# Optimization experiments

Hardware: AMD Instinct MI355X
Metric: run time of the kernel (lower is better)

The kernel has to match this reference:

```python
import jax, jax.numpy as jnp
import numpy as np

B, C_I, C_O, K, H, W = 8, 64, 64, 3, 256, 256
GROUPS = 16  # int(c_o / min(4, c_o)) = 64/4
EPS = 1e-5
PAD = K  # pad_x = pad_y = k + (bc-1) with bc_x=bc_y=1, k=3


def _conv(x, w):
    # x: (B, C_i, h, w), w: (C_o, C_i, K, K), valid conv, stride 1
    return jax.lax.conv_general_dilated(
        x, w, window_strides=(1, 1), padding='VALID',
        dimension_numbers=('NCHW', 'OIHW', 'NCHW'))


def setup_inputs() -> dict:
    key = jax.random.key(0)
    ks = jax.random.split(key, 10)
    s = 1.0 / np.sqrt(C_I * K * K)  # torch Conv2d default init bound
    wshape = (C_O, C_I, K, K)
    names = ['w_int', 'w_tl', 'w_tr', 'w_bl', 'w_br', 'w_top', 'w_bot', 'w_left', 'w_right']
    d = {'x': jax.random.normal(ks[0], (B, C_I, H, W), dtype=jnp.float32)}
    for i, n in enumerate(names):
        d[n] = jax.random.uniform(ks[i + 1], wshape, jnp.float32, -s, s)
    d['bias'] = jnp.zeros((1, C_O, 1, 1), jnp.float32)   # learnable_bias (init zeros)
    d['gamma'] = jnp.ones((C_O,), jnp.float32)           # GroupNorm weight
    d['beta'] = jnp.zeros((C_O,), jnp.float32)           # GroupNorm bias
    return d


def reference(x, w_int, w_tl, w_tr, w_bl, w_br, w_top, w_bot, w_left, w_right, bias, gamma, beta):
    p = PAD
    # corners -> (B,C,1,1)
    tl = _conv(x[:, :, :p, :p], w_tl)
    tr = _conv(x[:, :, :p, -p:], w_tr)
    bl = _conv(x[:, :, -p:, :p], w_bl)
    br = _conv(x[:, :, -p:, -p:], w_br)
    # edges -> (B,C,1,W-2) / (B,C,H-2,1)
    top = _conv(x[:, :, :p, :], w_top)
    bot = _conv(x[:, :, -p:, :], w_bot)
    left = _conv(x[:, :, :, :p], w_left)
    right = _conv(x[:, :, :, -p:], w_right)
    # interior -> (B,C,H-2,W-2)
    mid = _conv(x, w_int)
    mid = jnp.concatenate([left, mid, right], axis=3)       # (B,C,H-2,W)
    top_row = jnp.concatenate([tl, top, tr], axis=3)        # (B,C,1,W)
    bot_row = jnp.concatenate([bl, bot, br], axis=3)        # (B,C,1,W)
    # NOTE: original code puts the 'bottom' conv output first along dim 2
    y = jnp.concatenate([bot_row, mid, top_row], axis=2) + bias  # (B,C,H,W)
    # GroupNorm(16, 64)
    yg = y.reshape(B, GROUPS, -1)
    mu = jnp.mean(yg, axis=2, keepdims=True)
    var = jnp.var(yg, axis=2, keepdims=True)
    yn = ((yg - mu) * jax.lax.rsqrt(var + EPS)).reshape(B, C_O, H, W)
    yn = yn * gamma[None, :, None, None] + beta[None, :, None, None]
    # SELU activation; dropout(rate=0) is identity
    return jax.nn.selu(yn)
```

## Files before the change

kernel.cpp:

```cpp
#include <hip/hip_runtime.h>

#define B_ 8
#define CI 64
#define CO 64
#define H_ 256
#define W_ 256
#define EPS_ 1e-5f

#define SELU_SCALE 1.0507009873554805f
#define SELU_SA    1.7580993408473766f

typedef __attribute__((ext_vector_type(8))) short short8;
typedef __attribute__((ext_vector_type(4))) float f32x4;
typedef unsigned int u32;

__device__ __forceinline__ unsigned short f2bf(float f) {
    unsigned int u = __float_as_uint(f);
    u = (u + 0x7fffu + ((u >> 16) & 1u)) >> 16;
    return (unsigned short)u;
}
__device__ __forceinline__ float bf2f(unsigned short h) {
    return __uint_as_float(((unsigned)h) << 16);
}
__device__ __forceinline__ float selu_f(float u) {
    return (u > 0.f) ? SELU_SCALE * u : SELU_SA * (__expf(u) - 1.f);
}
__device__ __forceinline__ void gload_lds16(const void* g, void* l) {
    __builtin_amdgcn_global_load_lds(
        (const __attribute__((address_space(1))) u32*)g,
        (__attribute__((address_space(3))) u32*)l, 16, 0, 0);
}

__global__ __launch_bounds__(256) void prepass_weights(
    const float* __restrict__ w_int,
    const float* __restrict__ w_bl, const float* __restrict__ w_br,
    const float* __restrict__ w_tl, const float* __restrict__ w_tr,
    const float* __restrict__ w_bot, const float* __restrict__ w_top,
    const float* __restrict__ w_left, const float* __restrict__ w_right,
    unsigned short* __restrict__ wpre9, float* __restrict__ wedge)
{
    const int blk = blockIdx.x, t = threadIdx.x;
    const int wid = blk / 9, pos = blk % 9;
    const float* src = (wid == 0) ? w_bl : (wid == 1) ? w_br
                     : (wid == 2) ? w_tl : (wid == 3) ? w_tr
                     : (wid == 4) ? w_bot : (wid == 5) ? w_top
                     : (wid == 6) ? w_left : (wid == 7) ? w_right : w_int;
    for (int k = 0; k < 16; ++k) {
        const int lin = k * 256 + t;
        const int co = lin >> 6, cip = lin & 63;
        const int ci = cip ^ ((co & 7) << 3);
        wpre9[(size_t)wid * 36864 + pos * 4096 + lin] = f2bf(src[(co * 64 + ci) * 9 + pos]);
        if (wid < 8) {
            const int c4 = lin >> 8, co2 = (lin >> 2) & 63, j = lin & 3;
            const int ci2 = c4 * 4 + j;
            wedge[(size_t)wid * 36864 + pos * 4096 + lin] = src[(co2 * 64 + ci2) * 9 + pos];
        }
    }
}

__global__ __launch_bounds__(256) void prepass_x(
    const float* __restrict__ x, unsigned short* __restrict__ xpre)
{
    __shared__ unsigned short ls[256 * 72];
    const int row = blockIdx.x, b = blockIdx.y;
    const int t = threadIdx.x;
    const int colq = t >> 2;
    const float* xb = x + ((size_t)(b * 64) * 256 + row) * 256;

    for (int sp = 0; sp < 4; ++sp) {
        const int cibase = sp * 16 + (t & 3) * 4;
        float4 v[4];
#pragma unroll
        for (int e = 0; e < 4; ++e)
            v[e] = *(const float4*)(xb + (size_t)(cibase + e) * 65536 + colq * 4);
#pragma unroll
        for (int jj = 0; jj < 4; ++jj) {
            const int col = colq * 4 + jj;
            const int sw  = (col & 7) << 3;
            ushort4 pk;
            pk.x = f2bf((&v[0].x)[jj]);
            pk.y = f2bf((&v[1].x)[jj]);
            pk.z = f2bf((&v[2].x)[jj]);
            pk.w = f2bf((&v[3].x)[jj]);
            *(ushort4*)&ls[col * 72 + (cibase ^ sw)] = pk;
        }
    }
    __syncthreads();
    unsigned short* xp = xpre + ((size_t)(b * 256 + row)) * 256 * 64;
    for (int q = 0; q < 8; ++q) {
        const int lin = q * 256 + t;
        const int col = lin >> 3, k = lin & 7;
        *(uint4*)(xp + col * 64 + k * 8) = *(const uint4*)&ls[col * 72 + k * 8];
    }
}

__global__ __launch_bounds__(512, 4) void conv_mfma(
    const unsigned short* __restrict__ xpre, const unsigned short* __restrict__ wpre,
    const float* __restrict__ bias, unsigned short* __restrict__ ybf,
    float* __restrict__ part)
{
    __shared__ unsigned short xs[10 * 40 * 64];
    __shared__ unsigned short wl3[3][4096];
    __shared__ float sred[8][16][2];
    const int t = threadIdx.x, w = t >> 6, lane = t & 63;
    const int b = blockIdx.z, r0 = blockIdx.y * 8, c0 = blockIdx.x * 32;

    for (int L = w; L < 50; L += 8) {
        const int j = L / 5, i = L % 5;
        int rr = r0 - 1 + j; rr = rr < 0 ? 0 : (rr > 255 ? 255 : rr);
        int col = c0 - 2 + i * 8 + (lane >> 3);
        col = col < 0 ? 0 : (col > 255 ? 255 : col);
        const char* src = (const char*)xpre +
            ((size_t)((b * 256 + rr) * 256 + col)) * 128 + (lane & 7) * 16;
        gload_lds16(src, (char*)xs + j * 5120 + i * 1024);
    }
    gload_lds16((const char*)wpre + 0 * 8192 + w * 1024 + lane * 16,
                (char*)wl3[0] + w * 1024);
    gload_lds16((const char*)wpre + 1 * 8192 + w * 1024 + lane * 16,
                (char*)wl3[1] + w * 1024);

    const int l15 = lane & 15, lg = lane >> 4;
    const int sw15 = (l15 & 7) << 3;

    int jb[3];
#pragma unroll
    for (int kr = 0; kr < 3; ++kr) jb[kr] = (w + kr) * 5120;
    int offb[3][2][2];
#pragma unroll
    for (int kc = 0; kc < 3; ++kc)
#pragma unroll
        for (int n = 0; n < 2; ++n) {
            const int s = n * 16 + l15 + kc + 1;
#pragma unroll
            for (int ks = 0; ks < 2; ++ks) {
                const int cib = ks * 32 + lg * 8;
                offb[kc][n][ks] = s * 128 + ((cib ^ (((s + 6) & 7) << 3)) << 1);
            }
        }
    int afo[2][4];
#pragma unroll
    for (int ks = 0; ks < 2; ++ks)
#pragma unroll
        for (int m = 0; m < 4; ++m) {
            const int cib = ks * 32 + lg * 8;
            afo[ks][m] = (m * 16 + l15) * 128 + ((cib ^ sw15) << 1);
        }

    f32x4 acc[4][2];
#pragma unroll
    for (int m = 0; m < 4; ++m)
#pragma unroll
        for (int n = 0; n < 2; ++n)
            acc[m][n] = (f32x4){0.f, 0.f, 0.f, 0.f};

#pragma unroll
    for (int pos = 0; pos < 9; ++pos) {
        if (pos < 8) asm volatile("s_waitcnt vmcnt(1)" ::: "memory");
        else         asm volatile("s_waitcnt vmcnt(0)" ::: "memory");
        __builtin_amdgcn_s_barrier();
        __builtin_amdgcn_sched_barrier(0);
        if (pos + 2 <= 8)
            gload_lds16((const char*)wpre + (pos + 2) * 8192 + w * 1024 + lane * 16,
                        (char*)wl3[(pos + 2) % 3] + w * 1024);
        const int kr = pos / 3, kc = pos % 3;
        const char* wbuf = (const char*)wl3[pos % 3];
#pragma unroll
        for (int ks = 0; ks < 2; ++ks) {
            short8 bf[2], af[4];
#pragma unroll
            for (int n = 0; n < 2; ++n)
                bf[n] = *(const short8*)((const char*)xs + jb[kr] + offb[kc][n][ks]);
#pragma unroll
            for (int m = 0; m < 4; ++m)
                af[m] = *(const short8*)(wbuf + afo[ks][m]);
            __builtin_amdgcn_s_setprio(1);
#pragma unroll
            for (int m = 0; m < 4; ++m)
#pragma unroll
                for (int n = 0; n < 2; ++n)
                    acc[m][n] = __builtin_amdgcn_mfma_f32_16x16x32_bf16(
                        af[m], bf[n], acc[m][n], 0, 0, 0);
            __builtin_amdgcn_s_setprio(0);
        }
    }

    const int r = r0 + w;
    const bool rmask = (r != 0) && (r != 255);
    float s4[4] = {0.f, 0.f, 0.f, 0.f}, q4[4] = {0.f, 0.f, 0.f, 0.f};
#pragma unroll
    for (int m = 0; m < 4; ++m)
#pragma unroll
        for (int n = 0; n < 2; ++n) {
            const int c = c0 + n * 16 + l15;
            const bool pmask = rmask && (c != 0) && (c != 255);
#pragma unroll
            for (int reg = 0; reg < 4; ++reg) {
                const int co = m * 16 + lg * 4 + reg;
                const float v = acc[m][n][reg] + bias[co];
                ybf[(((size_t)b * 64 + co) * 256 + r) * 256 + c] = f2bf(v);
                if (pmask) { s4[m] += v; q4[m] += v * v; }
            }
        }
#pragma unroll
    for (int off = 1; off < 16; off <<= 1)
#pragma unroll
        for (int m = 0; m < 4; ++m) {
            s4[m] += __shfl_xor(s4[m], off);
            q4[m] += __shfl_xor(q4[m], off);
        }
    if (l15 == 0) {
#pragma unroll
        for (int m = 0; m < 4; ++m) {
            sred[w][m * 4 + lg][0] = s4[m];
            sred[w][m * 4 + lg][1] = q4[m];
        }
    }
    __syncthreads();
    if (t < 32) {
        const int g = t & 15, sel = t >> 4;
        float v = 0.f;
#pragma unroll
        for (int ww = 0; ww < 8; ++ww) v += sred[ww][g][sel];
        const int slot = blockIdx.y * 8 + blockIdx.x;
        part[((size_t)(b * 512 + slot) * 16 + g) * 2 + sel] = v;
    }
}

__global__ __launch_bounds__(256) void conv_edge_tb(
    const unsigned short* __restrict__ xpre, const unsigned short* __restrict__ wpre9,
    const float* __restrict__ bias, unsigned short* __restrict__ ybf,
    float* __restrict__ part)
{
    __shared__ unsigned short xs3[3 * 40 * 64];
    __shared__ unsigned short wl3[3][4096];
    __shared__ float ered[16][2];
    const int t = threadIdx.x, w = t >> 6, lane = t & 63;
    const int seg = blockIdx.x, edge = blockIdx.y, b = blockIdx.z;
    const int c0 = seg * 32;
    const int wid = 4 + edge;

    for (int L = w; L < 15; L += 4) {
        const int j = L / 5, i = L % 5;
        const int rr = (edge == 0) ? (253 + j) : j;
        int col = c0 - 2 + i * 8 + (lane >> 3);
        col = col < 0 ? 0 : (col > 255 ? 255 : col);
        gload_lds16((const char*)xpre +
                        ((size_t)((b * 256 + rr) * 256 + col)) * 128 + (lane & 7) * 16,
                    (char*)xs3 + j * 5120 + i * 1024);
    }
    const char* wsrc = (const char*)wpre9 + (size_t)wid * 73728;
#pragma unroll
    for (int c = 0; c < 2; ++c)
        gload_lds16(wsrc + 0 * 8192 + (w * 2 + c) * 1024 + lane * 16,
                    (char*)wl3[0] + (w * 2 + c) * 1024);
#pragma unroll
    for (int c = 0; c < 2; ++c)
        gload_lds16(wsrc + 1 * 8192 + (w * 2 + c) * 1024 + lane * 16,
                    (char*)wl3[1] + (w * 2 + c) * 1024);

    const int l15 = lane & 15, lg = lane >> 4;
    const int sw15 = (l15 & 7) << 3;
    int offb[3][2][2];
#pragma unroll
    for (int kc = 0; kc < 3; ++kc)
#pragma unroll
        for (int n = 0; n < 2; ++n) {
            const int s = n * 16 + l15 + kc + 1;
#pragma unroll
            for (int ks = 0; ks < 2; ++ks) {
                const int cib = ks * 32 + lg * 8;
                offb[kc][n][ks] = s * 128 + ((cib ^ (((s + 6) & 7) << 3)) << 1);
            }
        }
    int afo[2];
#pragma unroll
    for (int ks = 0; ks < 2; ++ks) {
        const int cib = ks * 32 + lg * 8;
        afo[ks] = (w * 16 + l15) * 128 + ((cib ^ sw15) << 1);
    }

    f32x4 acc[2];
    acc[0] = (f32x4){0.f, 0.f, 0.f, 0.f};
    acc[1] = (f32x4){0.f, 0.f, 0.f, 0.f};

#pragma unroll
    for (int pos = 0; pos < 9; ++pos) {
        if (pos < 8) asm volatile("s_waitcnt vmcnt(2)" ::: "memory");
        else         asm volatile("s_waitcnt vmcnt(0)" ::: "memory");
        __builtin_amdgcn_s_barrier();
        __builtin_amdgcn_sched_barrier(0);
        if (pos + 2 <= 8) {
#pragma unroll
            for (int c = 0; c < 2; ++c)
                gload_lds16(wsrc + (pos + 2) * 8192 + (w * 2 + c) * 1024 + lane * 16,
                            (char*)wl3[(pos + 2) % 3] + (w * 2 + c) * 1024);
        }
        const int kr = pos / 3, kc = pos % 3;
        const char* wbuf = (const char*)wl3[pos % 3];
#pragma unroll
        for (int ks = 0; ks < 2; ++ks) {
            short8 bf[2];
#pragma unroll
            for (int n = 0; n < 2; ++n)
                bf[n] = *(const short8*)((const char*)xs3 + kr * 5120 + offb[kc][n][ks]);
            const short8 af = *(const short8*)(wbuf + afo[ks]);
#pragma unroll
            for (int n = 0; n < 2; ++n)
                acc[n] = __builtin_amdgcn_mfma_f32_16x16x32_bf16(af, bf[n], acc[n], 0, 0, 0);
        }
    }

    const int r_out = (edge == 0) ? 0 : 255;
    float s = 0.f, q = 0.f;
#pragma unroll
    for (int n = 0; n < 2; ++n) {
        const int c = c0 + n * 16 + l15;
        const bool pmask = (c != 0) && (c != 255);
#pragma unroll
        for (int reg = 0; reg < 4; ++reg) {
            const int co = w * 16 + lg * 4 + reg;
            const float v = acc[n][reg] + bias[co];
            ybf[(((size_t)b * 64 + co) * 256 + r_out) * 256 + c] = f2bf(v);
            if (pmask) { s += v; q += v * v; }
        }
    }
    s += __shfl_xor(s, 1); q += __shfl_xor(q, 1);
    s += __shfl_xor(s, 2); q += __shfl_xor(q, 2);
    s += __shfl_xor(s, 4); q += __shfl_xor(q, 4);
    s += __shfl_xor(s, 8); q += __shfl_xor(q, 8);
    if (l15 == 0) { ered[w * 4 + lg][0] = s; ered[w * 4 + lg][1] = q; }
    __syncthreads();
    if (t < 32) {
        const int g = t & 15, sel = t >> 4;
        const int slot = 256 + edge * 8 + seg;
        part[((size_t)(b * 512 + slot) * 16 + g) * 2 + sel] = ered[g][sel];
    }
}

__global__ __launch_bounds__(256) void conv_edge_lr(
    const unsigned short* __restrict__ xpre, const unsigned short* __restrict__ wpre9,
    const float* __restrict__ bias, unsigned short* __restrict__ ybf,
    float* __restrict__ part)
{
    __shared__ unsigned short xr[66 * 200];
    __shared__ unsigned short wl3[3][4096];
    __shared__ float ered[16][2];
    const int t = threadIdx.x, w = t >> 6, lane = t & 63;
    const int seg = blockIdx.x, edge = blockIdx.y, b = blockIdx.z;
    const int r0 = seg * 64;
    const int wid = 6 + edge;
    const int colbase = edge ? 253 : 0;

    for (int u = t; u < 1584; u += 256) {
        const int row = u / 24, rem = u % 24;
        const int cl = rem >> 3, sub = rem & 7;
        int rr = r0 - 1 + row; rr = rr < 0 ? 0 : (rr > 255 ? 255 : rr);
        const int col = colbase + cl;
        const uint4 v = *(const uint4*)(xpre +
            ((size_t)((b * 256 + rr) * 256 + col)) * 64 + sub * 8);
        *(uint4*)((char*)xr + row * 400 + cl * 128 + sub * 16) = v;
    }
    const char* wsrc = (const char*)wpre9 + (size_t)wid * 73728;
#pragma unroll
    for (int c = 0; c < 2; ++c)
        gload_lds16(wsrc + 0 * 8192 + (w * 2 + c) * 1024 + lane * 16,
                    (char*)wl3[0] + (w * 2 + c) * 1024);
#pragma unroll
    for (int c = 0; c < 2; ++c)
        gload_lds16(wsrc + 1 * 8192 + (w * 2 + c) * 1024 + lane * 16,
                    (char*)wl3[1] + (w * 2 + c) * 1024);
    asm volatile("s_waitcnt lgkmcnt(0)" ::: "memory");

    const int l15 = lane & 15, lg = lane >> 4;
    const int sw15 = (l15 & 7) << 3;
    int offlr[3][2];
#pragma unroll
    for (int kc = 0; kc < 3; ++kc) {
        const int key = (colbase + kc) & 7;
#pragma unroll
        for (int ks = 0; ks < 2; ++ks) {
            const int cib = ks * 32 + lg * 8;
            offlr[kc][ks] = kc * 128 + ((cib ^ (key << 3)) << 1);
        }
    }
    int rowb[4];
#pragma unroll
    for (int n = 0; n < 4; ++n) rowb[n] = (n * 16 + l15) * 400;
    int afo[2];
#pragma unroll
    for (int ks = 0; ks < 2; ++ks) {
        const int cib = ks * 32 + lg * 8;
        afo[ks] = (w * 16 + l15) * 128 + ((cib ^ sw15) << 1);
    }

    f32x4 acc[4];
#pragma unroll
    for (int n = 0; n < 4; ++n) acc[n] = (f32x4){0.f, 0.f, 0.f, 0.f};

#pragma unroll
    for (int pos = 0; pos < 9; ++pos) {
        if (pos < 8) asm volatile("s_waitcnt vmcnt(2)" ::: "memory");
        else         asm volatile("s_waitcnt vmcnt(0)" ::: "memory");
        __builtin_amdgcn_s_barrier();
        __builtin_amdgcn_sched_barrier(0);
        if (pos + 2 <= 8) {
#pragma unroll
            for (int c = 0; c < 2; ++c)
                gload_lds16(wsrc + (pos + 2) * 8192 + (w * 2 + c) * 1024 + lane * 16,
                            (char*)wl3[(pos + 2) % 3] + (w * 2 + c) * 1024);
        }
        const int kr = pos / 3, kc = pos % 3;
        const char* wbuf = (const char*)wl3[pos % 3];
#pragma unroll
        for (int ks = 0; ks < 2; ++ks) {
            const short8 af = *(const short8*)(wbuf + afo[ks]);
#pragma unroll
            for (int n = 0; n < 4; ++n) {
                const short8 bf = *(const short8*)((const char*)xr +
                                    rowb[n] + kr * 400 + offlr[kc][ks]);
                acc[n] = __builtin_amdgcn_mfma_f32_16x16x32_bf16(af, bf, acc[n], 0, 0, 0);
            }
        }
    }

    const int c_out = edge ? 255 : 0;
    float s = 0.f, q = 0.f;
#pragma unroll
    for (int n = 0; n < 4; ++n) {
        const int r = r0 + n * 16 + l15;
        const bool pmask = (r != 0) && (r != 255);
#pragma unroll
        for (int reg = 0; reg < 4; ++reg) {
            const int co = w * 16 + lg * 4 + reg;
            const float v = acc[n][reg] + bias[co];
            ybf[(((size_t)b * 64 + co) * 256 + r) * 256 + c_out] = f2bf(v);
            if (pmask) { s += v; q += v * v; }
        }
    }
    s += __shfl_xor(s, 1); q += __shfl_xor(q, 1);
    s += __shfl_xor(s, 2); q += __shfl_xor(q, 2);
    s += __shfl_xor(s, 4); q += __shfl_xor(q, 4);
    s += __shfl_xor(s, 8); q += __shfl_xor(q, 8);
    if (l15 == 0) { ered[w * 4 + lg][0] = s; ered[w * 4 + lg][1] = q; }
    __syncthreads();
    if (t < 32) {
        const int g = t & 15, sel = t >> 4;
        const int slot = 272 + edge * 4 + seg;
        part[((size_t)(b * 512 + slot) * 16 + g) * 2 + sel] = ered[g][sel];
    }
}

__global__ __launch_bounds__(256) void conv_corner3(
    const unsigned short* __restrict__ xpre, const float* __restrict__ wedge,
    const float* __restrict__ bias, unsigned short* __restrict__ ybf,
    float* __restrict__ part)
{
    __shared__ float cred[4][16][2];
    const int b = blockIdx.x, t = threadIdx.x;
    const int corner = t >> 6, co = t & 63;
    const int wid  = corner;
    const int row0 = (corner < 2) ? 253 : 0;
    const int col0 = (corner & 1) ? 253 : 0;
    const int r_out = (corner < 2) ? 0 : 255;
    const int c_out = (corner & 1) ? 255 : 0;

    const float* wbase = wedge + (size_t)wid * 36864;
    float a0 = 0.f, a1 = 0.f, a2 = 0.f, a3 = 0.f;
#pragma unroll 1
    for (int pos = 0; pos < 9; ++pos) {
        const int kr = pos / 3, kc = pos % 3;
        const int row = row0 + kr, col = col0 + kc;
        const unsigned short* xp = xpre + ((size_t)((b * 256 + row) * 256 + col)) * 64;
        const int sw = (col & 7) << 3;
#pragma unroll
        for (int c4 = 0; c4 < 16; ++c4) {
            const float4 wv = *(const float4*)(wbase + pos * 4096 + c4 * 256 + co * 4);
            const ushort4 xv = *(const ushort4*)(xp + ((c4 * 4) ^ sw));
            a0 = fmaf(wv.x, bf2f(xv.x), a0);
            a1 = fmaf(wv.y, bf2f(xv.y), a1);
            a2 = fmaf(wv.z, bf2f(xv.z), a2);
            a3 = fmaf(wv.w, bf2f(xv.w), a3);
        }
    }
    const float v = (a0 + a1) + (a2 + a3) + bias[co];
    ybf[(((size_t)b * 64 + co) * 256 + r_out) * 256 + c_out] = f2bf(v);
    float s = v, q = v * v;
    s += __shfl_xor(s, 1); q += __shfl_xor(q, 1);
    s += __shfl_xor(s, 2); q += __shfl_xor(q, 2);
    if ((co & 3) == 0) { cred[corner][co >> 2][0] = s; cred[corner][co >> 2][1] = q; }
    __syncthreads();
    if (t < 32) {
        const int g = t & 15, sel = t >> 4;
        const float r = cred[0][g][sel] + cred[1][g][sel] +
                        cred[2][g][sel] + cred[3][g][sel];
        part[((size_t)(b * 512 + 280) * 16 + g) * 2 + sel] = r;
    }
}

__global__ __launch_bounds__(256) void stats_reduce(
    const float* __restrict__ part, float* __restrict__ mv)
{
    __shared__ float sred[16][16][2];
    const int b = blockIdx.x, t = threadIdx.x;
    const int g = t & 15, chunk = t >> 4;
    float s = 0.f, q = 0.f;
    for (int k = 0; k < 18; ++k) {
        const int slot = chunk * 18 + k;
        if (slot < 281) {
            const size_t base = ((size_t)(b * 512 + slot) * 16 + g) * 2;
            s += part[base]; q += part[base + 1];
        }
    }
    sred[chunk][g][0] = s; sred[chunk][g][1] = q;
    __syncthreads();
    if (t < 16) {
        float S = 0.f, Q = 0.f;
#pragma unroll
        for (int c = 0; c < 16; ++c) { S += sred[c][t][0]; Q += sred[c][t][1]; }
        const float inv_n = 1.0f / (4.0f * 65536.0f);
        const float mean = S * inv_n;
        const float var  = Q * inv_n - mean * mean;
        mv[(b * 16 + t) * 2]     = mean;
        mv[(b * 16 + t) * 2 + 1] = rsqrtf(var + EPS_);
    }
}

__global__ __launch_bounds__(256) void norm_bf(
    const unsigned short* __restrict__ ybf, float* __restrict__ out,
    const float* __restrict__ mv,
    const float* __restrict__ gamma, const float* __restrict__ beta)
{
    const size_t tt = (size_t)blockIdx.x * 256 + threadIdx.x;
    const size_t e = tt * 8;
    const int b  = (int)(e >> 22);
    const int ch = (int)((e >> 16) & 63);
    const int g  = ch >> 2;
    const float mean = mv[(b * 16 + g) * 2];
    const float rstd = mv[(b * 16 + g) * 2 + 1];
    const float ga = gamma[ch] * rstd;
    const float be = beta[ch] - mean * ga;

    const uint4 v = *(const uint4*)(ybf + e);
    float f[8];
    f[0] = __uint_as_float(v.x << 16); f[1] = __uint_as_float(v.x & 0xffff0000u);
    f[2] = __uint_as_float(v.y << 16); f[3] = __uint_as_float(v.y & 0xffff0000u);
    f[4] = __uint_as_float(v.z << 16); f[5] = __uint_as_float(v.z & 0xffff0000u);
    f[6] = __uint_as_float(v.w << 16); f[7] = __uint_as_float(v.w & 0xffff0000u);
    float4 o0, o1;
    o0.x = selu_f(f[0] * ga + be); o0.y = selu_f(f[1] * ga + be);
    o0.z = selu_f(f[2] * ga + be); o0.w = selu_f(f[3] * ga + be);
    o1.x = selu_f(f[4] * ga + be); o1.y = selu_f(f[5] * ga + be);
    o1.z = selu_f(f[6] * ga + be); o1.w = selu_f(f[7] * ga + be);
    *(float4*)(out + e)     = o0;
    *(float4*)(out + e + 4) = o1;
}

__global__ __launch_bounds__(256) void conv_main(
    const float* __restrict__ x, const float* __restrict__ w,
    const float* __restrict__ bias, float* __restrict__ y)
{
    const int c = threadIdx.x;
    const int r = blockIdx.x;
    const int b = blockIdx.y;
    const int rr = (r == 0) ? (H_ - 3) : ((r == H_ - 1) ? 0 : (r - 1));
    const int cc = min(max(c - 1, 0), W_ - 3);
    float acc[CO];
#pragma unroll
    for (int co = 0; co < CO; ++co) acc[co] = 0.f;
    const float* xb = x + (size_t)b * CI * H_ * W_;
    for (int ci = 0; ci < CI; ++ci) {
        const float* xp = xb + ((size_t)ci * H_ + rr) * W_ + cc;
        float xv[9];
#pragma unroll
        for (int kr = 0; kr < 3; ++kr)
#pragma unroll
            for (int kc = 0; kc < 3; ++kc)
                xv[kr * 3 + kc] = xp[kr * W_ + kc];
        const float* wci = w + ci * 9;
// ... 119 lines not shown
    }
#pragma unroll
    for (int off = 32; off; off >>= 1) {
        s += __shfl_down(s, off);
        q += __shfl_down(q, off);
    }
    __shared__ float red[8];
    const int wid = threadIdx.x >> 6;
    if ((threadIdx.x & 63) == 0) { red[wid * 2] = s; red[wid * 2 + 1] = q; }
    __syncthreads();
    if (threadIdx.x == 0) {
        ws[bid * 2]     = red[0] + red[2] + red[4] + red[6];
        ws[bid * 2 + 1] = red[1] + red[3] + red[5] + red[7];
    }
}

__global__ __launch_bounds__(256) void norm_stats(
    float* __restrict__ y, const float* __restrict__ st,
    const float* __restrict__ gamma, const float* __restrict__ beta)
{
    const size_t t = (size_t)blockIdx.x * 256 + threadIdx.x;
    const size_t e = t * 4;
    const int b  = (int)(e >> 22);
    const int ch = (int)((e >> 16) & 63);
    const int g  = ch >> 2;
    const int sb = ((b * 16 + g) * 4) * 2;
    const float S = st[sb] + st[sb + 2] + st[sb + 4] + st[sb + 6];
    const float Q = st[sb + 1] + st[sb + 3] + st[sb + 5] + st[sb + 7];
    const float inv_n = 1.0f / (4.0f * H_ * W_);
    const float mean  = S * inv_n;
    const float var   = Q * inv_n - mean * mean;
    const float rstd  = rsqrtf(var + EPS_);
    const float ga = gamma[ch] * rstd;
    const float be = beta[ch] - mean * ga;
    float4 v = reinterpret_cast<float4*>(y)[t];
    float u;
    u = v.x * ga + be; v.x = selu_f(u);
    u = v.y * ga + be; v.y = selu_f(u);
    u = v.z * ga + be; v.z = selu_f(u);
    u = v.w * ga + be; v.w = selu_f(u);
    reinterpret_cast<float4*>(y)[t] = v;
}

extern "C" void kernel_launch(void* const* d_in, const int* in_sizes, int n_in,
                              void* d_out, int out_size, void* d_ws, size_t ws_size,
                              hipStream_t stream) {
    const float* x       = (const float*)d_in[0];
    const float* w_int   = (const float*)d_in[1];
    const float* w_tl    = (const float*)d_in[2];
    const float* w_tr    = (const float*)d_in[3];
    const float* w_bl    = (const float*)d_in[4];
    const float* w_br    = (const float*)d_in[5];
    const float* w_top   = (const float*)d_in[6];
    const float* w_bot   = (const float*)d_in[7];
    const float* w_left  = (const float*)d_in[8];
    const float* w_right = (const float*)d_in[9];
    const float* bias    = (const float*)d_in[10];
    const float* gamma   = (const float*)d_in[11];
    const float* beta    = (const float*)d_in[12];

    float* out = (float*)d_out;

    const size_t XPRE  = 67108864ull;
    const size_t YBF   = 67108864ull;
    const size_t WPRE9 = 663552ull;
    const size_t WEDGE = 1179648ull;
    const size_t PART  = 524288ull;
    const size_t MV    = 1024ull;
    const size_t NEED  = XPRE + YBF + WPRE9 + WEDGE + PART + MV;

    if (ws_size >= NEED) {
        char* base = (char*)d_ws;
        unsigned short* xpre  = (unsigned short*)base;  base += XPRE;
        unsigned short* ybf   = (unsigned short*)base;  base += YBF;
        unsigned short* wpre9 = (unsigned short*)base;  base += WPRE9;
        float*          wedge = (float*)base;           base += WEDGE;
        float*          part  = (float*)base;           base += PART;
        float*          mv    = (float*)base;

        prepass_weights<<<dim3(81), 256, 0, stream>>>(
            w_int, w_bl, w_br, w_tl, w_tr, w_bot, w_top, w_left, w_right,
            wpre9, wedge);
        prepass_x<<<dim3(256, 8), 256, 0, stream>>>(x, xpre);
        conv_mfma<<<dim3(8, 32, 8), 512, 0, stream>>>(
            xpre, wpre9 + 8 * 36864, bias, ybf, part);
        conv_edge_tb<<<dim3(8, 2, 8), 256, 0, stream>>>(xpre, wpre9, bias, ybf, part);
        conv_edge_lr<<<dim3(4, 2, 8), 256, 0, stream>>>(xpre, wpre9, bias, ybf, part);
        conv_corner3<<<dim3(8), 256, 0, stream>>>(xpre, wedge, bias, ybf, part);
        stats_reduce<<<dim3(8), 256, 0, stream>>>(part, mv);
        norm_bf<<<dim3(16384), 256, 0, stream>>>(ybf, out, mv, gamma, beta);
    } else {
        float* stats = (float*)d_ws;
        conv_main<<<dim3(H_, B_), 256, 0, stream>>>(x, w_int, bias, out);
        conv_edge<<<dim3(B_, 4, 4), 256, 0, stream>>>(x, w_bot, w_top, w_left, w_right, bias, out);
        conv_corner<<<dim3(B_), 256, 0, stream>>>(x, w_bl, w_br, w_tl, w_tr, bias, out);
        stats_kernel<<<dim3(512), 256, 0, stream>>>(out, stats);
        norm_stats<<<dim3(32768), 256, 0, stream>>>(out, stats, gamma, beta);
    }
}
```

Measured before the change: 196.7 us.

## Fuse interior, edge and corner convolutions into a single launch

```diff
diff --git a/kernel.cpp b/kernel.cpp
--- a/kernel.cpp
+++ b/kernel.cpp
@@ -94,406 +94,364 @@
     }
 }
 
-__global__ __launch_bounds__(512, 4) void conv_mfma(
-    const unsigned short* __restrict__ xpre, const unsigned short* __restrict__ wpre,
-    const float* __restrict__ bias, unsigned short* __restrict__ ybf,
-    float* __restrict__ part)
+__global__ __launch_bounds__(512, 4) void conv_all(
+    const unsigned short* __restrict__ xpre, const unsigned short* __restrict__ wpre9,
+    const float* __restrict__ wedge, const float* __restrict__ bias,
+    unsigned short* __restrict__ ybf, float* __restrict__ part)
 {
     __shared__ unsigned short xs[10 * 40 * 64];
     __shared__ unsigned short wl3[3][4096];
     __shared__ float sred[8][16][2];
     const int t = threadIdx.x, w = t >> 6, lane = t & 63;
-    const int b = blockIdx.z, r0 = blockIdx.y * 8, c0 = blockIdx.x * 32;
-
-    for (int L = w; L < 50; L += 8) {
-        const int j = L / 5, i = L % 5;
-        int rr = r0 - 1 + j; rr = rr < 0 ? 0 : (rr > 255 ? 255 : rr);
-        int col = c0 - 2 + i * 8 + (lane >> 3);
-        col = col < 0 ? 0 : (col > 255 ? 255 : col);
-        const char* src = (const char*)xpre +
-            ((size_t)((b * 256 + rr) * 256 + col)) * 128 + (lane & 7) * 16;
-        gload_lds16(src, (char*)xs + j * 5120 + i * 1024);
-    }
-    gload_lds16((const char*)wpre + 0 * 8192 + w * 1024 + lane * 16,
-                (char*)wl3[0] + w * 1024);
-    gload_lds16((const char*)wpre + 1 * 8192 + w * 1024 + lane * 16,
-                (char*)wl3[1] + w * 1024);
-
+    const int b = blockIdx.z;
     const int l15 = lane & 15, lg = lane >> 4;
     const int sw15 = (l15 & 7) << 3;
 
-    int jb[3];
-#pragma unroll
-    for (int kr = 0; kr < 3; ++kr) jb[kr] = (w + kr) * 5120;
-    int offb[3][2][2];
-#pragma unroll
-    for (int kc = 0; kc < 3; ++kc)
-#pragma unroll
-        for (int n = 0; n < 2; ++n) {
-            const int s = n * 16 + l15 + kc + 1;
+    if (blockIdx.y < 32) {
+        const unsigned short* wpre = wpre9 + 8 * 36864;
+        const int r0 = blockIdx.y * 8, c0 = blockIdx.x * 32;
+
+        for (int L = w; L < 50; L += 8) {
+            const int j = L / 5, i = L % 5;
+            int rr = r0 - 1 + j; rr = rr < 0 ? 0 : (rr > 255 ? 255 : rr);
+            int col = c0 - 2 + i * 8 + (lane >> 3);
+            col = col < 0 ? 0 : (col > 255 ? 255 : col);
+            gload_lds16((const char*)xpre +
+                            ((size_t)((b * 256 + rr) * 256 + col)) * 128 + (lane & 7) * 16,
+                        (char*)xs + j * 5120 + i * 1024);
+        }
+        gload_lds16((const char*)wpre + 0 * 8192 + w * 1024 + lane * 16,
+                    (char*)wl3[0] + w * 1024);
+        gload_lds16((const char*)wpre + 1 * 8192 + w * 1024 + lane * 16,
+                    (char*)wl3[1] + w * 1024);
+
+        int jb[3];
+#pragma unroll
+        for (int kr = 0; kr < 3; ++kr) jb[kr] = (w + kr) * 5120;
+        int offb[3][2][2];
+#pragma unroll
+        for (int kc = 0; kc < 3; ++kc)
+#pragma unroll
+            for (int n = 0; n < 2; ++n) {
+                const int s = n * 16 + l15 + kc + 1;
+#pragma unroll
+                for (int ks = 0; ks < 2; ++ks) {
+                    const int cib = ks * 32 + lg * 8;
+                    offb[kc][n][ks] = s * 128 + ((cib ^ (((s + 6) & 7) << 3)) << 1);
+                }
+            }
+        int afo[2][4];
+#pragma unroll
+        for (int ks = 0; ks < 2; ++ks)
+#pragma unroll
+            for (int m = 0; m < 4; ++m) {
+                const int cib = ks * 32 + lg * 8;
+                afo[ks][m] = (m * 16 + l15) * 128 + ((cib ^ sw15) << 1);
+            }
+
+        f32x4 acc[4][2];
+#pragma unroll
+        for (int m = 0; m < 4; ++m)
+#pragma unroll
+            for (int n = 0; n < 2; ++n)
+                acc[m][n] = (f32x4){0.f, 0.f, 0.f, 0.f};
+
+#pragma unroll
+        for (int pos = 0; pos < 9; ++pos) {
+            if (pos < 8) asm volatile("s_waitcnt vmcnt(1)" ::: "memory");
+            else         asm volatile("s_waitcnt vmcnt(0)" ::: "memory");
+            __builtin_amdgcn_s_barrier();
+            __builtin_amdgcn_sched_barrier(0);
+            if (pos + 2 <= 8)
+                gload_lds16((const char*)wpre + (pos + 2) * 8192 + w * 1024 + lane * 16,
+                            (char*)wl3[(pos + 2) % 3] + w * 1024);
+            const int kr = pos / 3, kc = pos % 3;
+            const char* wbuf = (const char*)wl3[pos % 3];
+#pragma unroll
+            for (int ks = 0; ks < 2; ++ks) {
+                short8 bf[2], af[4];
+#pragma unroll
+                for (int n = 0; n < 2; ++n)
+                    bf[n] = *(const short8*)((const char*)xs + jb[kr] + offb[kc][n][ks]);
+#pragma unroll
+                for (int m = 0; m < 4; ++m)
+                    af[m] = *(const short8*)(wbuf + afo[ks][m]);
+                __builtin_amdgcn_s_setprio(1);
+#pragma unroll
+                for (int m = 0; m < 4; ++m)
+#pragma unroll
+                    for (int n = 0; n < 2; ++n)
+                        acc[m][n] = __builtin_amdgcn_mfma_f32_16x16x32_bf16(
+                            af[m], bf[n], acc[m][n], 0, 0, 0);
+                __builtin_amdgcn_s_setprio(0);
+            }
+        }
+
+        const int r = r0 + w;
+        const bool rmask = (r != 0) && (r != 255);
+        float s4[4] = {0.f, 0.f, 0.f, 0.f}, q4[4] = {0.f, 0.f, 0.f, 0.f};
+#pragma unroll
+        for (int m = 0; m < 4; ++m)
+#pragma unroll
+            for (int n = 0; n < 2; ++n) {
+                const int c = c0 + n * 16 + l15;
+                const bool pmask = rmask && (c != 0) && (c != 255);
+#pragma unroll
+                for (int reg = 0; reg < 4; ++reg) {
+                    const int co = m * 16 + lg * 4 + reg;
+                    const float v = acc[m][n][reg] + bias[co];
+                    if (pmask) {
+                        ybf[(((size_t)b * 64 + co) * 256 + r) * 256 + c] = f2bf(v);
+                        s4[m] += v; q4[m] += v * v;
+                    }
+                }
+            }
+#pragma unroll
+        for (int off = 1; off < 16; off <<= 1)
+#pragma unroll
+            for (int m = 0; m < 4; ++m) {
+                s4[m] += __shfl_xor(s4[m], off);
+                q4[m] += __shfl_xor(q4[m], off);
+            }
+        if (l15 == 0) {
+#pragma unroll
+            for (int m = 0; m < 4; ++m) {
+                sred[w][m * 4 + lg][0] = s4[m];
+                sred[w][m * 4 + lg][1] = q4[m];
+            }
+        }
+        __syncthreads();
+        if (t < 32) {
+            const int g = t & 15, sel = t >> 4;
+            float v = 0.f;
+#pragma unroll
+            for (int ww = 0; ww < 8; ++ww) v += sred[ww][g][sel];
+            const int slot = blockIdx.y * 8 + blockIdx.x;
+            part[((size_t)(b * 512 + slot) * 16 + g) * 2 + sel] = v;
+        }
+        return;
+    }
+
+    const int job = (blockIdx.y - 32) * 8 + blockIdx.x;
+    if (job > 24) return;
+
+    if (job < 16) {
+        const int edge = job >> 3, seg = job & 7;
+        const int c0 = seg * 32;
+        const char* wsrc = (const char*)wpre9 + (size_t)(4 + edge) * 73728;
+        for (int L = w; L < 15; L += 8) {
+            const int j = L / 5, i = L % 5;
+            const int rr = (edge == 0) ? (253 + j) : j;
+            int col = c0 - 2 + i * 8 + (lane >> 3);
+            col = col < 0 ? 0 : (col > 255 ? 255 : col);
+            gload_lds16((const char*)xpre +
+                            ((size_t)((b * 256 + rr) * 256 + col)) * 128 + (lane & 7) * 16,
+                        (char*)xs + j * 5120 + i * 1024);
+        }
+        gload_lds16(wsrc + 0 * 8192 + w * 1024 + lane * 16, (char*)wl3[0] + w * 1024);
+        gload_lds16(wsrc + 1 * 8192 + w * 1024 + lane * 16, (char*)wl3[1] + w * 1024);
+
+        const int cot = w & 3, nh = w >> 2;
+        int offb2[3][2];
+#pragma unroll
+        for (int kc = 0; kc < 3; ++kc) {
+            const int s = nh * 16 + l15 + kc + 1;
 #pragma unroll
             for (int ks = 0; ks < 2; ++ks) {
                 const int cib = ks * 32 + lg * 8;
-                offb[kc][n][ks] = s * 128 + ((cib ^ (((s + 6) & 7) << 3)) << 1);
-            }
-        }
-    int afo[2][4];
-#pragma unroll
-    for (int ks = 0; ks < 2; ++ks)
-#pragma unroll
-        for (int m = 0; m < 4; ++m) {
+                offb2[kc][ks] = s * 128 + ((cib ^ (((s + 6) & 7) << 3)) << 1);
+            }
+        }
+        int afo2[2];
+#pragma unroll
+        for (int ks = 0; ks < 2; ++ks) {
             const int cib = ks * 32 + lg * 8;
-            afo[ks][m] = (m * 16 + l15) * 128 + ((cib ^ sw15) << 1);
-        }
-
-    f32x4 acc[4][2];
-#pragma unroll
-    for (int m = 0; m < 4; ++m)
-#pragma unroll
-        for (int n = 0; n < 2; ++n)
-            acc[m][n] = (f32x4){0.f, 0.f, 0.f, 0.f};
-
-#pragma unroll
-    for (int pos = 0; pos < 9; ++pos) {
-        if (pos < 8) asm volatile("s_waitcnt vmcnt(1)" ::: "memory");
-        else         asm volatile("s_waitcnt vmcnt(0)" ::: "memory");
-        __builtin_amdgcn_s_barrier();
-        __builtin_amdgcn_sched_barrier(0);
-        if (pos + 2 <= 8)
-            gload_lds16((const char*)wpre + (pos + 2) * 8192 + w * 1024 + lane * 16,
-                        (char*)wl3[(pos + 2) % 3] + w * 1024);
-        const int kr = pos / 3, kc = pos % 3;
-        const char* wbuf = (const char*)wl3[pos % 3];
-#pragma unroll
-        for (int ks = 0; ks < 2; ++ks) {
-            short8 bf[2], af[4];
-#pragma unroll
-            for (int n = 0; n < 2; ++n)
-                bf[n] = *(const short8*)((const char*)xs + jb[kr] + offb[kc][n][ks]);
-#pragma unroll
-            for (int m = 0; m < 4; ++m)
-                af[m] = *(const short8*)(wbuf + afo[ks][m]);
-            __builtin_amdgcn_s_setprio(1);
-#pragma unroll
-            for (int m = 0; m < 4; ++m)
-#pragma unroll
-                for (int n = 0; n < 2; ++n)
-                    acc[m][n] = __builtin_amdgcn_mfma_f32_16x16x32_bf16(
-                        af[m], bf[n], acc[m][n], 0, 0, 0);
-            __builtin_amdgcn_s_setprio(0);
-        }
-    }
-
-    const int r = r0 + w;
-    const bool rmask = (r != 0) && (r != 255);
-    float s4[4] = {0.f, 0.f, 0.f, 0.f}, q4[4] = {0.f, 0.f, 0.f, 0.f};
-#pragma unroll
-    for (int m = 0; m < 4; ++m)
-#pragma unroll
-        for (int n = 0; n < 2; ++n) {
-            const int c = c0 + n * 16 + l15;
-            const bool pmask = rmask && (c != 0) && (c != 255);
-#pragma unroll
-            for (int reg = 0; reg < 4; ++reg) {
-                const int co = m * 16 + lg * 4 + reg;
-                const float v = acc[m][n][reg] + bias[co];
-                ybf[(((size_t)b * 64 + co) * 256 + r) * 256 + c] = f2bf(v);
-                if (pmask) { s4[m] += v; q4[m] += v * v; }
-            }
-        }
-#pragma unroll
-    for (int off = 1; off < 16; off <<= 1)
-#pragma unroll
-        for (int m = 0; m < 4; ++m) {
-            s4[m] += __shfl_xor(s4[m], off);
-            q4[m] += __shfl_xor(q4[m], off);
-        }
-    if (l15 == 0) {
-#pragma unroll
-        for (int m = 0; m < 4; ++m) {
-            sred[w][m * 4 + lg][0] = s4[m];
-            sred[w][m * 4 + lg][1] = q4[m];
-        }
-    }
-    __syncthreads();
-    if (t < 32) {
-        const int g = t & 15, sel = t >> 4;
-        float v = 0.f;
-#pragma unroll
-        for (int ww = 0; ww < 8; ++ww) v += sred[ww][g][sel];
-        const int slot = blockIdx.y * 8 + blockIdx.x;
-        part[((size_t)(b * 512 + slot) * 16 + g) * 2 + sel] = v;
-    }
-}
-
-__global__ __launch_bounds__(256) void conv_edge_tb(
-    const unsigned short* __restrict__ xpre, const unsigned short* __restrict__ wpre9,
-    const float* __restrict__ bias, unsigned short* __restrict__ ybf,
-    float* __restrict__ part)
-{
-    __shared__ unsigned short xs3[3 * 40 * 64];
-    __shared__ unsigned short wl3[3][4096];
-    __shared__ float ered[16][2];
-    const int t = threadIdx.x, w = t >> 6, lane = t & 63;
-    const int seg = blockIdx.x, edge = blockIdx.y, b = blockIdx.z;
-    const int c0 = seg * 32;
-    const int wid = 4 + edge;
-
-    for (int L = w; L < 15; L += 4) {
-        const int j = L / 5, i = L % 5;
-        const int rr = (edge == 0) ? (253 + j) : j;
-        int col = c0 - 2 + i * 8 + (lane >> 3);
-        col = col < 0 ? 0 : (col > 255 ? 255 : col);
-        gload_lds16((const char*)xpre +
-                        ((size_t)((b * 256 + rr) * 256 + col)) * 128 + (lane & 7) * 16,
-                    (char*)xs3 + j * 5120 + i * 1024);
-    }
-    const char* wsrc = (const char*)wpre9 + (size_t)wid * 73728;
-#pragma unroll
-    for (int c = 0; c < 2; ++c)
-        gload_lds16(wsrc + 0 * 8192 + (w * 2 + c) * 1024 + lane * 16,
-                    (char*)wl3[0] + (w * 2 + c) * 1024);
-#pragma unroll
-    for (int c = 0; c < 2; ++c)
-        gload_lds16(wsrc + 1 * 8192 + (w * 2 + c) * 1024 + lane * 16,
-                    (char*)wl3[1] + (w * 2 + c) * 1024);
-
-    const int l15 = lane & 15, lg = lane >> 4;
-    const int sw15 = (l15 & 7) << 3;
-    int offb[3][2][2];
-#pragma unroll
-    for (int kc = 0; kc < 3; ++kc)
-#pragma unroll
-        for (int n = 0; n < 2; ++n) {
-            const int s = n * 16 + l15 + kc + 1;
+            afo2[ks] = (cot * 16 + l15) * 128 + ((cib ^ sw15) << 1);
+        }
+        f32x4 acc0 = (f32x4){0.f, 0.f, 0.f, 0.f};
+
+#pragma unroll
+        for (int pos = 0; pos < 9; ++pos) {
+            if (pos < 8) asm volatile("s_waitcnt vmcnt(1)" ::: "memory");
+            else         asm volatile("s_waitcnt vmcnt(0)" ::: "memory");
+            __builtin_amdgcn_s_barrier();
+            __builtin_amdgcn_sched_barrier(0);
+            if (pos + 2 <= 8)
+                gload_lds16(wsrc + (pos + 2) * 8192 + w * 1024 + lane * 16,
+                            (char*)wl3[(pos + 2) % 3] + w * 1024);
+            const int kr = pos / 3, kc = pos % 3;
+            const char* wbuf = (const char*)wl3[pos % 3];
+#pragma unroll
+            for (int ks = 0; ks < 2; ++ks) {
+                const short8 bf = *(const short8*)((const char*)xs + kr * 5120 + offb2[kc][ks]);
+                const short8 af = *(const short8*)(wbuf + afo2[ks]);
+                acc0 = __builtin_amdgcn_mfma_f32_16x16x32_bf16(af, bf, acc0, 0, 0, 0);
+            }
+        }
+
+        const int r_out = edge ? 255 : 0;
+        const int c = c0 + nh * 16 + l15;
+        const bool pmask = (c != 0) && (c != 255);
+        float s = 0.f, q = 0.f;
+#pragma unroll
+        for (int reg = 0; reg < 4; ++reg) {
+            const int co = cot * 16 + lg * 4 + reg;
+            const float v = acc0[reg] + bias[co];
+            if (pmask) {
+                ybf[(((size_t)b * 64 + co) * 256 + r_out) * 256 + c] = f2bf(v);
+                s += v; q += v * v;
+            }
+        }
+        s += __shfl_xor(s, 1); q += __shfl_xor(q, 1);
+        s += __shfl_xor(s, 2); q += __shfl_xor(q, 2);
+        s += __shfl_xor(s, 4); q += __shfl_xor(q, 4);
+        s += __shfl_xor(s, 8); q += __shfl_xor(q, 8);
+        float* sb = (float*)sred;
+        if (l15 == 0) { sb[(w * 4 + lg) * 2] = s; sb[(w * 4 + lg) * 2 + 1] = q; }
+        __syncthreads();
+        if (t < 32) {
+            const int g = t & 15, sel = t >> 4;
+            const int ct = g >> 2, sub = g & 3;
+            const float v = sb[(ct * 4 + sub) * 2 + sel] + sb[((ct + 4) * 4 + sub) * 2 + sel];
+            part[((size_t)(b * 512 + 256 + job) * 16 + g) * 2 + sel] = v;
+        }
+    } else if (job < 24) {
+        const int jj = job - 16;
+        const int edge = jj >> 2, seg = jj & 3;
+        const int r0 = seg * 64;
+        const int colbase = edge ? 253 : 0;
+        unsigned short* xr = xs;
+        for (int u = t; u < 1584; u += 512) {
+            const int row = u / 24, rem = u % 24;
+            const int cl = rem >> 3, sub = rem & 7;
+            int rr = r0 - 1 + row; rr = rr < 0 ? 0 : (rr > 255 ? 255 : rr);
+            const int col = colbase + cl;
+            const uint4 v = *(const uint4*)(xpre +
+                ((size_t)((b * 256 + rr) * 256 + col)) * 64 + sub * 8);
+            *(uint4*)((char*)xr + row * 400 + cl * 128 + sub * 16) = v;
+        }
+        const char* wsrc = (const char*)wpre9 + (size_t)(6 + edge) * 73728;
+        gload_lds16(wsrc + 0 * 8192 + w * 1024 + lane * 16, (char*)wl3[0] + w * 1024);
+        gload_lds16(wsrc + 1 * 8192 + w * 1024 + lane * 16, (char*)wl3[1] + w * 1024);
+        asm volatile("s_waitcnt lgkmcnt(0)" ::: "memory");
+
+        const int cot = w & 3, np = w >> 2;
+        int offlr[3][2];
+#pragma unroll
+        for (int kc = 0; kc < 3; ++kc) {
+            const int key = (colbase + kc) & 7;
 #pragma unroll
             for (int ks = 0; ks < 2; ++ks) {
                 const int cib = ks * 32 + lg * 8;
-                offb[kc][n][ks] = s * 128 + ((cib ^ (((s + 6) & 7) << 3)) << 1);
-            }
-        }
-    int afo[2];
-#pragma unroll
-    for (int ks = 0; ks < 2; ++ks) {
-        const int cib = ks * 32 + lg * 8;
-        afo[ks] = (w * 16 + l15) * 128 + ((cib ^ sw15) << 1);
-    }
-
-    f32x4 acc[2];
-    acc[0] = (f32x4){0.f, 0.f, 0.f, 0.f};
-    acc[1] = (f32x4){0.f, 0.f, 0.f, 0.f};
-
-#pragma unroll
-    for (int pos = 0; pos < 9; ++pos) {
-        if (pos < 8) asm volatile("s_waitcnt vmcnt(2)" ::: "memory");
-        else         asm volatile("s_waitcnt vmcnt(0)" ::: "memory");
-        __builtin_amdgcn_s_barrier();
-        __builtin_amdgcn_sched_barrier(0);
-        if (pos + 2 <= 8) {
-#pragma unroll
-            for (int c = 0; c < 2; ++c)
-                gload_lds16(wsrc + (pos + 2) * 8192 + (w * 2 + c) * 1024 + lane * 16,
-                            (char*)wl3[(pos + 2) % 3] + (w * 2 + c) * 1024);
-        }
-        const int kr = pos / 3, kc = pos % 3;
-        const char* wbuf = (const char*)wl3[pos % 3];
-#pragma unroll
-        for (int ks = 0; ks < 2; ++ks) {
-            short8 bf[2];
-#pragma unroll
-            for (int n = 0; n < 2; ++n)
-                bf[n] = *(const short8*)((const char*)xs3 + kr * 5120 + offb[kc][n][ks]);
-            const short8 af = *(const short8*)(wbuf + afo[ks]);
-#pragma unroll
-            for (int n = 0; n < 2; ++n)
-                acc[n] = __builtin_amdgcn_mfma_f32_16x16x32_bf16(af, bf[n], acc[n], 0, 0, 0);
-        }
-    }
-
-    const int r_out = (edge == 0) ? 0 : 255;
-    float s = 0.f, q = 0.f;
-#pragma unroll
-    for (int n = 0; n < 2; ++n) {
-        const int c = c0 + n * 16 + l15;
-        const bool pmask = (c != 0) && (c != 255);
-#pragma unroll
-        for (int reg = 0; reg < 4; ++reg) {
-            const int co = w * 16 + lg * 4 + reg;
-            const float v = acc[n][reg] + bias[co];
-            ybf[(((size_t)b * 64 + co) * 256 + r_out) * 256 + c] = f2bf(v);
-            if (pmask) { s += v; q += v * v; }
-        }
-    }
-    s += __shfl_xor(s, 1); q += __shfl_xor(q, 1);
-    s += __shfl_xor(s, 2); q += __shfl_xor(q, 2);
-    s += __shfl_xor(s, 4); q += __shfl_xor(q, 4);
-    s += __shfl_xor(s, 8); q += __shfl_xor(q, 8);
-    if (l15 == 0) { ered[w * 4 + lg][0] = s; ered[w * 4 + lg][1] = q; }
-    __syncthreads();
-    if (t < 32) {
-        const int g = t & 15, sel = t >> 4;
-        const int slot = 256 + edge * 8 + seg;
-        part[((size_t)(b * 512 + slot) * 16 + g) * 2 + sel] = ered[g][sel];
-    }
-}
-
-__global__ __launch_bounds__(256) void conv_edge_lr(
-    const unsigned short* __restrict__ xpre, const unsigned short* __restrict__ wpre9,
-    const float* __restrict__ bias, unsigned short* __restrict__ ybf,
-    float* __restrict__ part)
-{
-    __shared__ unsigned short xr[66 * 200];
-    __shared__ unsigned short wl3[3][4096];
-    __shared__ float ered[16][2];
-    const int t = threadIdx.x, w = t >> 6, lane = t & 63;
-    const int seg = blockIdx.x, edge = blockIdx.y, b = blockIdx.z;
-    const int r0 = seg * 64;
-    const int wid = 6 + edge;
-    const int colbase = edge ? 253 : 0;
-
-    for (int u = t; u < 1584; u += 256) {
-        const int row = u / 24, rem = u % 24;
-        const int cl = rem >> 3, sub = rem & 7;
-        int rr = r0 - 1 + row; rr = rr < 0 ? 0 : (rr > 255 ? 255 : rr);
-        const int col = colbase + cl;
-        const uint4 v = *(const uint4*)(xpre +
-            ((size_t)((b * 256 + rr) * 256 + col)) * 64 + sub * 8);
-        *(uint4*)((char*)xr + row * 400 + cl * 128 + sub * 16) = v;
-    }
-    const char* wsrc = (const char*)wpre9 + (size_t)wid * 73728;
-#pragma unroll
-    for (int c = 0; c < 2; ++c)
-        gload_lds16(wsrc + 0 * 8192 + (w * 2 + c) * 1024 + lane * 16,
-                    (char*)wl3[0] + (w * 2 + c) * 1024);
-#pragma unroll
-    for (int c = 0; c < 2; ++c)
-        gload_lds16(wsrc + 1 * 8192 + (w * 2 + c) * 1024 + lane * 16,
-                    (char*)wl3[1] + (w * 2 + c) * 1024);
-    asm volatile("s_waitcnt lgkmcnt(0)" ::: "memory");
-
-    const int l15 = lane & 15, lg = lane >> 4;
-    const int sw15 = (l15 & 7) << 3;
-    int offlr[3][2];
-#pragma unroll
-    for (int kc = 0; kc < 3; ++kc) {
-        const int key = (colbase + kc) & 7;
+                offlr[kc][ks] = kc * 128 + ((cib ^ (key << 3)) << 1);
+            }
+        }
+        int rowb2[2];
+#pragma unroll
+        for (int j = 0; j < 2; ++j) rowb2[j] = ((np * 2 + j) * 16 + l15) * 400;
+        int afo2[2];
 #pragma unroll
         for (int ks = 0; ks < 2; ++ks) {
             const int cib = ks * 32 + lg * 8;
-            offlr[kc][ks] = kc * 128 + ((cib ^ (key << 3)) << 1);
-        }
-    }
-    int rowb[4];
-#pragma unroll
-    for (int n = 0; n < 4; ++n) rowb[n] = (n * 16 + l15) * 400;
-    int afo[2];
-#pragma unroll
-    for (int ks = 0; ks < 2; ++ks) {
-        const int cib = ks * 32 + lg * 8;
-        afo[ks] = (w * 16 + l15) * 128 + ((cib ^ sw15) << 1);
-    }
-
-    f32x4 acc[4];
-#pragma unroll
-    for (int n = 0; n < 4; ++n) acc[n] = (f32x4){0.f, 0.f, 0.f, 0.f};
-
-#pragma unroll
-    for (int pos = 0; pos < 9; ++pos) {
-        if (pos < 8) asm volatile("s_waitcnt vmcnt(2)" ::: "memory");
-        else         asm volatile("s_waitcnt vmcnt(0)" ::: "memory");
-        __builtin_amdgcn_s_barrier();
-        __builtin_amdgcn_sched_barrier(0);
-        if (pos + 2 <= 8) {
-#pragma unroll
-            for (int c = 0; c < 2; ++c)
-                gload_lds16(wsrc + (pos + 2) * 8192 + (w * 2 + c) * 1024 + lane * 16,
-                            (char*)wl3[(pos + 2) % 3] + (w * 2 + c) * 1024);
-        }
-        const int kr = pos / 3, kc = pos % 3;
-        const char* wbuf = (const char*)wl3[pos % 3];
-#pragma unroll
-        for (int ks = 0; ks < 2; ++ks) {
-            const short8 af = *(const short8*)(wbuf + afo[ks]);
-#pragma unroll
-            for (int n = 0; n < 4; ++n) {
-                const short8 bf = *(const short8*)((const char*)xr +
-                                    rowb[n] + kr * 400 + offlr[kc][ks]);
-                acc[n] = __builtin_amdgcn_mfma_f32_16x16x32_bf16(af, bf, acc[n], 0, 0, 0);
-            }
-        }
-    }
-
-    const int c_out = edge ? 255 : 0;
-    float s = 0.f, q = 0.f;
-#pragma unroll
-    for (int n = 0; n < 4; ++n) {
-        const int r = r0 + n * 16 + l15;
-        const bool pmask = (r != 0) && (r != 255);
-#pragma unroll
-        for (int reg = 0; reg < 4; ++reg) {
-            const int co = w * 16 + lg * 4 + reg;
-            const float v = acc[n][reg] + bias[co];
-            ybf[(((size_t)b * 64 + co) * 256 + r) * 256 + c_out] = f2bf(v);
-            if (pmask) { s += v; q += v * v; }
-        }
-    }
-    s += __shfl_xor(s, 1); q += __shfl_xor(q, 1);
-    s += __shfl_xor(s, 2); q += __shfl_xor(q, 2);
-    s += __shfl_xor(s, 4); q += __shfl_xor(q, 4);
-    s += __shfl_xor(s, 8); q += __shfl_xor(q, 8);
-    if (l15 == 0) { ered[w * 4 + lg][0] = s; ered[w * 4 + lg][1] = q; }
-    __syncthreads();
-    if (t < 32) {
-        const int g = t & 15, sel = t >> 4;
-        const int slot = 272 + edge * 4 + seg;
-        part[((size_t)(b * 512 + slot) * 16 + g) * 2 + sel] = ered[g][sel];
-    }
-}
-
-__global__ __launch_bounds__(256) void conv_corner3(
-    const unsigned short* __restrict__ xpre, const float* __restrict__ wedge,
-    const float* __restrict__ bias, unsigned short* __restrict__ ybf,
-    float* __restrict__ part)
-{
-    __shared__ float cred[4][16][2];
-    const int b = blockIdx.x, t = threadIdx.x;
-    const int corner = t >> 6, co = t & 63;
-    const int wid  = corner;
-    const int row0 = (corner < 2) ? 253 : 0;
-    const int col0 = (corner & 1) ? 253 : 0;
-    const int r_out = (corner < 2) ? 0 : 255;
-    const int c_out = (corner & 1) ? 255 : 0;
-
-    const float* wbase = wedge + (size_t)wid * 36864;
-    float a0 = 0.f, a1 = 0.f, a2 = 0.f, a3 = 0.f;
+            afo2[ks] = (cot * 16 + l15) * 128 + ((cib ^ sw15) << 1);
+        }
+        f32x4 accA = (f32x4){0.f, 0.f, 0.f, 0.f};
+        f32x4 accB = (f32x4){0.f, 0.f, 0.f, 0.f};
+
+#pragma unroll
+        for (int pos = 0; pos < 9; ++pos) {
+            if (pos < 8) asm volatile("s_waitcnt vmcnt(1)" ::: "memory");
+            else         asm volatile("s_waitcnt vmcnt(0)" ::: "memory");
+            __builtin_amdgcn_s_barrier();
+            __builtin_amdgcn_sched_barrier(0);
+            if (pos + 2 <= 8)
+                gload_lds16(wsrc + (pos + 2) * 8192 + w * 1024 + lane * 16,
+                            (char*)wl3[(pos + 2) % 3] + w * 1024);
+            const int kr = pos / 3, kc = pos % 3;
+            const char* wbuf = (const char*)wl3[pos % 3];
+#pragma unroll
+            for (int ks = 0; ks < 2; ++ks) {
+                const short8 af = *(const short8*)(wbuf + afo2[ks]);
+                const short8 bfA = *(const short8*)((const char*)xr + rowb2[0] + kr * 400 + offlr[kc][ks]);
+                const short8 bfB = *(const short8*)((const char*)xr + rowb2[1] + kr * 400 + offlr[kc][ks]);
+                accA = __builtin_amdgcn_mfma_f32_16x16x32_bf16(af, bfA, accA, 0, 0, 0);
+                accB = __builtin_amdgcn_mfma_f32_16x16x32_bf16(af, bfB, accB, 0, 0, 0);
+            }
+        }
+
+        const int c_out = edge ? 255 : 0;
+        float s = 0.f, q = 0.f;
+#pragma unroll
+        for (int j = 0; j < 2; ++j) {
+            const int r = r0 + (np * 2 + j) * 16 + l15;
+            const bool pmask = (r != 0) && (r != 255);
+            const f32x4 a = j ? accB : accA;
+#pragma unroll
+            for (int reg = 0; reg < 4; ++reg) {
+                const int co = cot * 16 + lg * 4 + reg;
+                const float v = a[reg] + bias[co];
+                if (pmask) {
+                    ybf[(((size_t)b * 64 + co) * 256 + r) * 256 + c_out] = f2bf(v);
+                    s += v; q += v * v;
+                }
+            }
+        }
+        s += __shfl_xor(s, 1); q += __shfl_xor(q, 1);
+        s += __shfl_xor(s, 2); q += __shfl_xor(q, 2);
+        s += __shfl_xor(s, 4); q += __shfl_xor(q, 4);
+        s += __shfl_xor(s, 8); q += __shfl_xor(q, 8);
+        float* sb = (float*)sred;
+        if (l15 == 0) { sb[(w * 4 + lg) * 2] = s; sb[(w * 4 + lg) * 2 + 1] = q; }
+        __syncthreads();
+        if (t < 32) {
+            const int g = t & 15, sel = t >> 4;
+            const int ct = g >> 2, sub = g & 3;
+            const float v = sb[(ct * 4 + sub) * 2 + sel] + sb[((ct + 4) * 4 + sub) * 2 + sel];
+            part[((size_t)(b * 512 + 272 + jj) * 16 + g) * 2 + sel] = v;
+        }
+    } else {
+        float* cred = (float*)sred;
+        if (w < 4) {
+            const int corner = w, co = lane;
+            const int row0 = (corner < 2) ? 253 : 0;
+            const int col0 = (corner & 1) ? 253 : 0;
+            const int r_out = (corner < 2) ? 0 : 255;
+            const int c_out = (corner & 1) ? 255 : 0;
+            const float* wbase = wedge + (size_t)corner * 36864;
+            float a0 = 0.f, a1 = 0.f, a2 = 0.f, a3 = 0.f;
 #pragma unroll 1
-    for (int pos = 0; pos < 9; ++pos) {
-        const int kr = pos / 3, kc = pos % 3;
-        const int row = row0 + kr, col = col0 + kc;
-        const unsigned short* xp = xpre + ((size_t)((b * 256 + row) * 256 + col)) * 64;
-        const int sw = (col & 7) << 3;
-#pragma unroll
-        for (int c4 = 0; c4 < 16; ++c4) {
-            const float4 wv = *(const float4*)(wbase + pos * 4096 + c4 * 256 + co * 4);
-            const ushort4 xv = *(const ushort4*)(xp + ((c4 * 4) ^ sw));
-            a0 = fmaf(wv.x, bf2f(xv.x), a0);
-            a1 = fmaf(wv.y, bf2f(xv.y), a1);
-            a2 = fmaf(wv.z, bf2f(xv.z), a2);
-            a3 = fmaf(wv.w, bf2f(xv.w), a3);
-        }
-    }
-    const float v = (a0 + a1) + (a2 + a3) + bias[co];
-    ybf[(((size_t)b * 64 + co) * 256 + r_out) * 256 + c_out] = f2bf(v);
-    float s = v, q = v * v;
-    s += __shfl_xor(s, 1); q += __shfl_xor(q, 1);
-    s += __shfl_xor(s, 2); q += __shfl_xor(q, 2);
-    if ((co & 3) == 0) { cred[corner][co >> 2][0] = s; cred[corner][co >> 2][1] = q; }
-    __syncthreads();
-    if (t < 32) {
-        const int g = t & 15, sel = t >> 4;
-        const float r = cred[0][g][sel] + cred[1][g][sel] +
-                        cred[2][g][sel] + cred[3][g][sel];
-        part[((size_t)(b * 512 + 280) * 16 + g) * 2 + sel] = r;
+            for (int pos = 0; pos < 9; ++pos) {
+                const int kr = pos / 3, kc = pos % 3;
+                const int row = row0 + kr, col = col0 + kc;
+                const unsigned short* xp = xpre + ((size_t)((b * 256 + row) * 256 + col)) * 64;
+                const int sw = (col & 7) << 3;
+#pragma unroll
+                for (int c4 = 0; c4 < 16; ++c4) {
+                    const float4 wv = *(const float4*)(wbase + pos * 4096 + c4 * 256 + co * 4);
+                    const ushort4 xv = *(const ushort4*)(xp + ((c4 * 4) ^ sw));
+                    a0 = fmaf(wv.x, bf2f(xv.x), a0);
+                    a1 = fmaf(wv.y, bf2f(xv.y), a1);
+                    a2 = fmaf(wv.z, bf2f(xv.z), a2);
+                    a3 = fmaf(wv.w, bf2f(xv.w), a3);
+                }
+            }
+            const float v = (a0 + a1) + (a2 + a3) + bias[co];
+            ybf[(((size_t)b * 64 + co) * 256 + r_out) * 256 + c_out] = f2bf(v);
+            float s = v, q = v * v;
+            s += __shfl_xor(s, 1); q += __shfl_xor(q, 1);
+            s += __shfl_xor(s, 2); q += __shfl_xor(q, 2);
+            if ((co & 3) == 0) {
+                cred[(corner * 16 + (co >> 2)) * 2]     = s;
+                cred[(corner * 16 + (co >> 2)) * 2 + 1] = q;
+            }
+        }
+        __syncthreads();
+        if (t < 32) {
+            const int g = t & 15, sel = t >> 4;
+            const float r = cred[(0 * 16 + g) * 2 + sel] + cred[(1 * 16 + g) * 2 + sel] +
+                            cred[(2 * 16 + g) * 2 + sel] + cred[(3 * 16 + g) * 2 + sel];
+            part[((size_t)(b * 512 + 280) * 16 + g) * 2 + sel] = r;
+        }
     }
 }
 
@@ -779,11 +737,8 @@
             w_int, w_bl, w_br, w_tl, w_tr, w_bot, w_top, w_left, w_right,
             wpre9, wedge);
         prepass_x<<<dim3(256, 8), 256, 0, stream>>>(x, xpre);
-        conv_mfma<<<dim3(8, 32, 8), 512, 0, stream>>>(
-            xpre, wpre9 + 8 * 36864, bias, ybf, part);
-        conv_edge_tb<<<dim3(8, 2, 8), 256, 0, stream>>>(xpre, wpre9, bias, ybf, part);
-        conv_edge_lr<<<dim3(4, 2, 8), 256, 0, stream>>>(xpre, wpre9, bias, ybf, part);
-        conv_corner3<<<dim3(8), 256, 0, stream>>>(xpre, wedge, bias, ybf, part);
+        conv_all<<<dim3(8, 36, 8), 512, 0, stream>>>(
+            xpre, wpre9, wedge, bias, ybf, part);
         stats_reduce<<<dim3(8), 256, 0, stream>>>(part, mv);
         norm_bf<<<dim3(16384), 256, 0, stream>>>(ybf, out, mv, gamma, beta);
     } else {
```

After: 172.4 us. -12.4%, faster.
